# Kernel tuning notes

Hardware: AMD Instinct MI355X
Metric: run time of the kernel (lower is better)

The kernel has to match this reference:

```python
import jax, jax.numpy as jnp
import numpy as np

B, D, T, K = 16, 512, 4096, 1024

def setup_inputs() -> dict:
    key = jax.random.key(0)
    kx, kc = jax.random.split(key)
    x = jax.random.normal(kx, (B, D, T), dtype=jnp.float32)
    codebook = jax.random.normal(kc, (K, D), dtype=jnp.float32)
    return {"x": x, "codebook": codebook}

def reference(x, codebook):
    # x: [B, D, T] -> xt: [B, T, D]
    xt = jnp.transpose(x, (0, 2, 1))
    x_sq = jnp.sum(xt * xt, axis=-1, keepdims=True)          # [B, T, 1]
    c_sq = jnp.sum(codebook * codebook, axis=-1)             # [K]
    cross = jnp.einsum('btd,kd->btk', xt, codebook)          # [B, T, K]
    dist = x_sq - 2.0 * cross + c_sq                         # [B, T, K]
    indexes = jnp.argmin(dist, axis=2)                       # [B, T] int
    quantized = codebook[indexes]                            # [B, T, D]
    quantized = jnp.transpose(quantized, (0, 2, 1))          # [B, D, T]
    return quantized, indexes
```

## Files before the change

kernel.cpp:

```cpp
#include <hip/hip_runtime.h>

#define BB 16
#define DD 512
#define TT 4096
#define KK 1024

typedef _Float16 h16;
typedef __attribute__((ext_vector_type(8))) _Float16 half8;
typedef __attribute__((ext_vector_type(4))) float float4v;

#define XTH_OFF 0ull
#define XTL_OFF 67108864ull
#define CBH_OFF 134217728ull
#define CBL_OFF 135266304ull
#define CSQ_OFF 136314880ull
#define WS_NEED (136314880ull + 4096ull)

#define GLOAD_LDS16(g, l) __builtin_amdgcn_global_load_lds( \
    (const __attribute__((address_space(1))) void*)(g),      \
    (__attribute__((address_space(3))) void*)(l), 16, 0, 0)

__global__ void csq_kernel(const float* __restrict__ cb, float* __restrict__ csq) {
    int wave = threadIdx.x >> 6;
    int lane = threadIdx.x & 63;
    int row  = blockIdx.x * 4 + wave;
    const float* r = cb + (size_t)row * DD;
    float s = 0.f;
    #pragma unroll
    for (int i = 0; i < DD / 64; ++i) { float v = r[lane + i * 64]; s += v * v; }
    #pragma unroll
    for (int off = 32; off; off >>= 1) s += __shfl_down(s, off, 64);
    if (lane == 0) csq[row] = s;
}

__global__ __launch_bounds__(256) void split_x_kernel(const float* __restrict__ x,
                                                      h16* __restrict__ xth,
                                                      h16* __restrict__ xtl) {
    __shared__ float xs[32][132];
    const int tb = blockIdx.x, dcb = blockIdx.y, b = blockIdx.z;
    const int tid = threadIdx.x;
    const int t0 = tb * 128, d0 = dcb * 32;
    const float* xp = x + ((size_t)b * DD + d0) * TT + t0;
    #pragma unroll
    for (int j = 0; j < 4; ++j) {
        int i4 = tid + 256 * j;
        int dd = i4 >> 5, c4 = (i4 & 31) << 2;
        *(float4*)&xs[dd][c4] = *(const float4*)(xp + (size_t)dd * TT + c4);
    }
    __syncthreads();
    const int r = tid >> 1;
    const int ch = (tid & 1) * 16;
    h16 hv[16], lv[16];
    #pragma unroll
    for (int i = 0; i < 16; ++i) {
        float v = xs[ch + i][r];
        h16 h = (h16)v;
        hv[i] = h;
        lv[i] = (h16)(v - (float)h);
    }
    size_t o = (((size_t)(b * 32 + tb) * 16) + dcb) * 4096 + (size_t)tid * 16;
    *(half8*)(xth + o)     = *(half8*)&hv[0];
    *(half8*)(xth + o + 8) = *(half8*)&hv[8];
    *(half8*)(xtl + o)     = *(half8*)&lv[0];
    *(half8*)(xtl + o + 8) = *(half8*)&lv[8];
}

__global__ __launch_bounds__(256) void split_cb_kernel(const float* __restrict__ cb,
                                                       h16* __restrict__ cbh,
                                                       h16* __restrict__ cbl) {
    const int kb = blockIdx.x >> 4, dcb = blockIdx.x & 15;
    const int tid = threadIdx.x;
    const float* cp = cb + ((size_t)kb * 128) * DD + dcb * 32;
    h16* oh = cbh + ((size_t)(kb * 16 + dcb)) * 4096;
    h16* ol = cbl + ((size_t)(kb * 16 + dcb)) * 4096;
    #pragma unroll
    for (int j = 0; j < 4; ++j) {
        int i4 = tid + 256 * j;
        int rr = i4 >> 3, c4 = (i4 & 7) << 2;
        float4 v = *(const float4*)(cp + (size_t)rr * DD + c4);
        float vv[4] = {v.x, v.y, v.z, v.w};
        h16 h[4], l[4];
        #pragma unroll
        for (int i = 0; i < 4; ++i) {
            h[i] = (h16)vv[i];
            l[i] = (h16)(vv[i] - (float)h[i]);
        }
        *(ushort4*)(oh + rr * 32 + c4) = *(ushort4*)h;
        *(ushort4*)(ol + rr * 32 + c4) = *(ushort4*)l;
    }
}

__global__ __launch_bounds__(256, 2) void mfma_argmin_kernel(
    const h16* __restrict__ xth, const h16* __restrict__ xtl,
    const h16* __restrict__ cbh, const h16* __restrict__ cbl,
    const float* __restrict__ csq, const float* __restrict__ cb,
    float* __restrict__ idx_f_out, float* __restrict__ out) {

    __shared__ h16 ash[2][4096];
    __shared__ h16 asl[2][4096];
    __shared__ h16 bsh[2][4096];
    __shared__ h16 bsl[2][4096];
    __shared__ float redv[2][128];
    __shared__ int   redi[2][128];

    const int tid = threadIdx.x;
    const int wid = tid >> 6, lane = tid & 63;
    const int wm = wid & 1, wn = wid >> 1;
    const int tb = blockIdx.x, b = blockIdx.y;
    const int t0 = tb * 128;
    const int c  = lane & 15;
    const int q  = lane >> 4;

    const h16* aH = xth + ((size_t)(b * 32 + tb) * 16) * 4096;
    const h16* aL = xtl + ((size_t)(b * 32 + tb) * 16) * 4096;

    const int soff0 = tid * 8;
    const int soff1 = soff0 + 2048;

    GLOAD_LDS16(aH + soff0,  &ash[0][soff0]);
    GLOAD_LDS16(aH + soff1,  &ash[0][soff1]);
    GLOAD_LDS16(aL + soff0,  &asl[0][soff0]);
    GLOAD_LDS16(aL + soff1,  &asl[0][soff1]);
    GLOAD_LDS16(cbh + soff0, &bsh[0][soff0]);
    GLOAD_LDS16(cbh + soff1, &bsh[0][soff1]);
    GLOAD_LDS16(cbl + soff0, &bsl[0][soff0]);
    GLOAD_LDS16(cbl + soff1, &bsl[0][soff1]);

    float best[16];
    int   bidx[16];
    #pragma unroll
    for (int i = 0; i < 16; ++i) { best[i] = 3.4e38f; bidx[i] = 0; }

    asm volatile("s_waitcnt vmcnt(0)\n\ts_barrier" ::: "memory");

    for (int kci = 0; kci < 8; ++kci) {
        float4v acc[4][4];
        #pragma unroll
        for (int m = 0; m < 4; ++m)
            #pragma unroll
            for (int n = 0; n < 4; ++n)
                acc[m][n] = (float4v){0.f, 0.f, 0.f, 0.f};

        for (int dcb = 0; dcb < 16; ++dcb) {
            const int g  = kci * 16 + dcb;
            const int bf = g & 1;

            if (g + 1 < 128) {
                const int gn = g + 1;
                const int kn = gn >> 4, dn = gn & 15;
                const int nb = bf ^ 1;
                const h16* aHs = aH + (size_t)dn * 4096;
                const h16* aLs = aL + (size_t)dn * 4096;
                const h16* bHs = cbh + ((size_t)(kn * 16 + dn)) * 4096;
                const h16* bLs = cbl + ((size_t)(kn * 16 + dn)) * 4096;
                GLOAD_LDS16(aHs + soff0, &ash[nb][soff0]);
                GLOAD_LDS16(aHs + soff1, &ash[nb][soff1]);
                GLOAD_LDS16(aLs + soff0, &asl[nb][soff0]);
                GLOAD_LDS16(aLs + soff1, &asl[nb][soff1]);
                GLOAD_LDS16(bHs + soff0, &bsh[nb][soff0]);
                GLOAD_LDS16(bHs + soff1, &bsh[nb][soff1]);
                GLOAD_LDS16(bLs + soff0, &bsl[nb][soff0]);
                GLOAD_LDS16(bLs + soff1, &bsl[nb][soff1]);
            }

            const int doff = q * 8;
            half8 Ah[4], Al[4], Bh[4], Bl[4];
            #pragma unroll
            for (int m = 0; m < 4; ++m) {
                int row = wm * 64 + m * 16 + c;
                Ah[m] = *(const half8*)(&ash[bf][row * 32 + doff]);
                Al[m] = *(const half8*)(&asl[bf][row * 32 + doff]);
            }
            #pragma unroll
            for (int n = 0; n < 4; ++n) {
                int row = wn * 64 + n * 16 + c;
                Bh[n] = *(const half8*)(&bsh[bf][row * 32 + doff]);
                Bl[n] = *(const half8*)(&bsl[bf][row * 32 + doff]);
            }

            __builtin_amdgcn_s_setprio(1);
            #pragma unroll
            for (int n = 0; n < 4; ++n)
                #pragma unroll
                for (int m = 0; m < 4; ++m)
                    acc[m][n] = __builtin_amdgcn_mfma_f32_16x16x32_f16(Ah[m], Bh[n], acc[m][n], 0, 0, 0);
            #pragma unroll
            for (int n = 0; n < 4; ++n)
                #pragma unroll
                for (int m = 0; m < 4; ++m)
                    acc[m][n] = __builtin_amdgcn_mfma_f32_16x16x32_f16(Ah[m], Bl[n], acc[m][n], 0, 0, 0);
            #pragma unroll
            for (int n = 0; n < 4; ++n)
                #pragma unroll
                for (int m = 0; m < 4; ++m)
                    acc[m][n] = __builtin_amdgcn_mfma_f32_16x16x32_f16(Al[m], Bh[n], acc[m][n], 0, 0, 0);
            __builtin_amdgcn_s_setprio(0);

            asm volatile("s_waitcnt vmcnt(0)\n\ts_barrier" ::: "memory");
        }

        #pragma unroll
        for (int n = 0; n < 4; ++n) {
            int kg = kci * 128 + wn * 64 + n * 16 + c;
            float cq = csq[kg];
            #pragma unroll
            for (int m = 0; m < 4; ++m)
                #pragma unroll
                for (int r = 0; r < 4; ++r) {
                    float s = fmaf(-2.0f, acc[m][n][r], cq);
                    int slot = m * 4 + r;
                    if (s < best[slot]) { best[slot] = s; bidx[slot] = kg; }
                }
        }
    }

    #pragma unroll
    for (int slot = 0; slot < 16; ++slot) {
        float v = best[slot]; int i = bidx[slot];
        #pragma unroll
        for (int d = 1; d < 16; d <<= 1) {
            float pv = __shfl_xor(v, d);
            int   pi = __shfl_xor(i, d);
            if (pv < v || (pv == v && pi < i)) { v = pv; i = pi; }
        }
        if (c == 0) {
            int m = slot >> 2, r = slot & 3;
            int tl = wm * 64 + m * 16 + q * 4 + r;
            redv[wn][tl] = v; redi[wn][tl] = i;
        }
    }
    __syncthreads();
    if (tid < 128) {
        float v0 = redv[0][tid]; int i0 = redi[0][tid];
        float v1 = redv[1][tid]; int i1 = redi[1][tid];
        if (v1 < v0 || (v1 == v0 && i1 < i0)) { v0 = v1; i0 = i1; }
        idx_f_out[(size_t)b * TT + t0 + tid] = (float)i0;
        redi[0][tid] = i0;
    }
    __syncthreads();

    const int tl = tid & 127, dg = tid >> 7;
    const int k = redi[0][tl];
    const float* row = cb + (size_t)k * DD + dg * 256;
    float* ob = out + ((size_t)b * DD + dg * 256) * TT + t0 + tl;
    #pragma unroll 4
    for (int i = 0; i < 64; ++i) {
        float4 v = *(const float4*)(row + i * 4);
        ob[(size_t)(i * 4 + 0) * TT] = v.x;
        ob[(size_t)(i * 4 + 1) * TT] = v.y;
        ob[(size_t)(i * 4 + 2) * TT] = v.z;
        ob[(size_t)(i * 4 + 3) * TT] = v.w;
    }
}

__global__ void gather_kernel(const float* __restrict__ cb,
                              const float* __restrict__ idx_f,
                              float* __restrict__ out) {
    int b  = blockIdx.y;
    int t  = blockIdx.x * 256 + threadIdx.x;
    int d0 = blockIdx.z * (DD / 4);
    int k  = (int)idx_f[(size_t)b * TT + t];
    const float* row = cb + (size_t)k * DD;
    float* ob = out + (size_t)b * DD * TT + t;
    #pragma unroll 8
    for (int d = d0; d < d0 + DD / 4; ++d)
        ob[(size_t)d * TT] = row[d];
}

__global__ __launch_bounds__(256) void argmin_fp32_kernel(
    const float* __restrict__ x, const float* __restrict__ cb,
    const float* __restrict__ csq, float* __restrict__ idx_f_out) {

    __shared__ float xs[32][128];
    __shared__ float cs[32][132];

    const int tid = threadIdx.x;
    const int b = blockIdx.y;
    const int t_blk = blockIdx.x * 128;
    const int tq = tid & 15, kq = tid >> 4;
    const int t0 = tq * 8, k0 = kq * 8;
    const float* xb = x + (size_t)b * DD * TT;

    float best[8]; int bidx[8];
    #pragma unroll
    for (int i = 0; i < 8; ++i) { best[i] = 3.4e38f; bidx[i] = 0; }

    for (int kc = 0; kc < KK; kc += 128) {
        float acc[8][8];
        #pragma unroll
        for (int i = 0; i < 8; ++i)
            #pragma unroll
            for (int j = 0; j < 8; ++j) acc[i][j] = 0.f;
        for (int dc = 0; dc < DD; dc += 32) {
            __syncthreads();
            #pragma unroll
            for (int j = 0; j < 4; ++j) {
                int i4 = tid + 256 * j;
                int dd = i4 >> 5, tp = (i4 & 31) << 2;
                *(float4*)&xs[dd][tp] =
                    *(const float4*)(xb + (size_t)(dc + dd) * TT + t_blk + tp);
            }
            #pragma unroll
            for (int j = 0; j < 4; ++j) {
                int i4 = tid + 256 * j;
                int kk = i4 >> 3, dq = (i4 & 7) << 2;
                float4 v = *(const float4*)(cb + (size_t)(kc + kk) * DD + dc + dq);
                cs[dq + 0][kk] = v.x; cs[dq + 1][kk] = v.y;
                cs[dq + 2][kk] = v.z; cs[dq + 3][kk] = v.w;
            }
            __syncthreads();
            #pragma unroll 8
            for (int dd = 0; dd < 32; ++dd) {
                float a[8], bv[8];
                *(float4*)&a[0]  = *(const float4*)&xs[dd][t0];
                *(float4*)&a[4]  = *(const float4*)&xs[dd][t0 + 4];
                *(float4*)&bv[0] = *(const float4*)&cs[dd][k0];
                *(float4*)&bv[4] = *(const float4*)&cs[dd][k0 + 4];
                #pragma unroll
                for (int i = 0; i < 8; ++i)
                    #pragma unroll
                    for (int j = 0; j < 8; ++j)
                        acc[i][j] = fmaf(a[i], bv[j], acc[i][j]);
            }
        }
        #pragma unroll
        for (int j = 0; j < 8; ++j) {
            int kg = kc + k0 + j;
            float cq = csq[kg];
            #pragma unroll
            for (int i = 0; i < 8; ++i) {
                float s = cq - 2.0f * acc[i][j];
                if (s < best[i]) { best[i] = s; bidx[i] = kg; }
            }
        }
    }
    __syncthreads();
    float* rbest = &xs[0][0];
    int*   ridx  = (int*)&cs[0][0];
    #pragma unroll
    for (int i = 0; i < 8; ++i) {
        rbest[kq * 128 + t0 + i] = best[i];
        ridx [kq * 128 + t0 + i] = bidx[i];
    }
    __syncthreads();
    if (tid < 128) {
        float bv = rbest[tid]; int bi = ridx[tid];
        #pragma unroll
        for (int g = 1; g < 16; ++g) {
            float v = rbest[g * 128 + tid]; int ii = ridx[g * 128 + tid];
            if (v < bv || (v == bv && ii < bi)) { bv = v; bi = ii; }
        }
        idx_f_out[(size_t)b * TT + t_blk + tid] = (float)bi;
    }
}

extern "C" void kernel_launch(void* const* d_in, const int* in_sizes, int n_in,
                              void* d_out, int out_size, void* d_ws, size_t ws_size,
                              hipStream_t stream) {
    const float* x  = (const float*)d_in[0];
    const float* cb = (const float*)d_in[1];
    float* out   = (float*)d_out;
    float* idx_f = out + (size_t)BB * DD * TT;

    if (ws_size >= WS_NEED) {
        h16* xth = (h16*)((char*)d_ws + XTH_OFF);
        h16* xtl = (h16*)((char*)d_ws + XTL_OFF);
        h16* cbh = (h16*)((char*)d_ws + CBH_OFF);
        h16* cbl = (h16*)((char*)d_ws + CBL_OFF);
        float* csq = (float*)((char*)d_ws + CSQ_OFF);

        csq_kernel<<<KK / 4, 256, 0, stream>>>(cb, csq);
        split_cb_kernel<<<128, 256, 0, stream>>>(cb, cbh, cbl);
        split_x_kernel<<<dim3(TT / 128, DD / 32, BB), 256, 0, stream>>>(x, xth, xtl);
        mfma_argmin_kernel<<<dim3(TT / 128, BB), 256, 0, stream>>>(
            xth, xtl, cbh, cbl, csq, cb, idx_f, out);
    } else {
        float* csq = (float*)d_ws;
        csq_kernel<<<KK / 4, 256, 0, stream>>>(cb, csq);
        argmin_fp32_kernel<<<dim3(TT / 128, BB), 256, 0, stream>>>(x, cb, csq, idx_f);
        gather_kernel<<<dim3(TT / 256, BB, 4), 256, 0, stream>>>(cb, idx_f, out);
    }
}
```

Baseline: 501.4 us.

## Use 8 waves per block with halved per-wave N tile and deeper prefetch

The argmin GEMM kernel now launches 512 threads (8 waves) per block, with each wave covering 32 codebook columns instead of 64. This halves accumulator registers and lets more waves hide latency. The LDS pipeline is reworked to prefetch two stages ahead, with partial vmcnt waits and barriers placed before the MFMA block. The final cross-wave argmin reduction grows to four groups, and the gather/transposed write is split across four d-groups. The risks are the extra barriers per stage, the lower MFMA work per LDS read, and the removal of setprio.

Result: faster. 488.8 us (-2.5%).

```diff
diff --git a/kernel.cpp b/kernel.cpp
--- a/kernel.cpp
+++ b/kernel.cpp
@@ -90,7 +90,7 @@
     }
 }
 
-__global__ __launch_bounds__(256, 2) void mfma_argmin_kernel(
+__global__ __launch_bounds__(512, 4) void mfma_argmin_kernel(
     const h16* __restrict__ xth, const h16* __restrict__ xtl,
     const h16* __restrict__ cbh, const h16* __restrict__ cbl,
     const float* __restrict__ csq, const float* __restrict__ cb,
@@ -100,12 +100,13 @@
     __shared__ h16 asl[2][4096];
     __shared__ h16 bsh[2][4096];
     __shared__ h16 bsl[2][4096];
-    __shared__ float redv[2][128];
-    __shared__ int   redi[2][128];
+    __shared__ float redv[4][128];
+    __shared__ int   redi[4][128];
 
     const int tid = threadIdx.x;
     const int wid = tid >> 6, lane = tid & 63;
-    const int wm = wid & 1, wn = wid >> 1;
+    const int wm = wid & 1;
+    const int wn = wid >> 1;
     const int tb = blockIdx.x, b = blockIdx.y;
     const int t0 = tb * 128;
     const int c  = lane & 15;
@@ -114,57 +115,40 @@
     const h16* aH = xth + ((size_t)(b * 32 + tb) * 16) * 4096;
     const h16* aL = xtl + ((size_t)(b * 32 + tb) * 16) * 4096;
 
-    const int soff0 = tid * 8;
-    const int soff1 = soff0 + 2048;
-
-    GLOAD_LDS16(aH + soff0,  &ash[0][soff0]);
-    GLOAD_LDS16(aH + soff1,  &ash[0][soff1]);
-    GLOAD_LDS16(aL + soff0,  &asl[0][soff0]);
-    GLOAD_LDS16(aL + soff1,  &asl[0][soff1]);
-    GLOAD_LDS16(cbh + soff0, &bsh[0][soff0]);
-    GLOAD_LDS16(cbh + soff1, &bsh[0][soff1]);
-    GLOAD_LDS16(cbl + soff0, &bsl[0][soff0]);
-    GLOAD_LDS16(cbl + soff1, &bsl[0][soff1]);
+    const int soff = tid * 8;
+
+    GLOAD_LDS16(aH  + soff,        &ash[0][soff]);
+    GLOAD_LDS16(aL  + soff,        &asl[0][soff]);
+    GLOAD_LDS16(cbh + soff,        &bsh[0][soff]);
+    GLOAD_LDS16(cbl + soff,        &bsl[0][soff]);
+    GLOAD_LDS16(aH  + 4096 + soff, &ash[1][soff]);
+    GLOAD_LDS16(aL  + 4096 + soff, &asl[1][soff]);
+    GLOAD_LDS16(cbh + 4096 + soff, &bsh[1][soff]);
+    GLOAD_LDS16(cbl + 4096 + soff, &bsl[1][soff]);
 
     float best[16];
     int   bidx[16];
     #pragma unroll
     for (int i = 0; i < 16; ++i) { best[i] = 3.4e38f; bidx[i] = 0; }
 
-    asm volatile("s_waitcnt vmcnt(0)\n\ts_barrier" ::: "memory");
-
     for (int kci = 0; kci < 8; ++kci) {
-        float4v acc[4][4];
+        float4v acc[4][2];
         #pragma unroll
         for (int m = 0; m < 4; ++m)
             #pragma unroll
-            for (int n = 0; n < 4; ++n)
+            for (int n = 0; n < 2; ++n)
                 acc[m][n] = (float4v){0.f, 0.f, 0.f, 0.f};
 
         for (int dcb = 0; dcb < 16; ++dcb) {
             const int g  = kci * 16 + dcb;
             const int bf = g & 1;
 
-            if (g + 1 < 128) {
-                const int gn = g + 1;
-                const int kn = gn >> 4, dn = gn & 15;
-                const int nb = bf ^ 1;
-                const h16* aHs = aH + (size_t)dn * 4096;
-                const h16* aLs = aL + (size_t)dn * 4096;
-                const h16* bHs = cbh + ((size_t)(kn * 16 + dn)) * 4096;
-                const h16* bLs = cbl + ((size_t)(kn * 16 + dn)) * 4096;
-                GLOAD_LDS16(aHs + soff0, &ash[nb][soff0]);
-                GLOAD_LDS16(aHs + soff1, &ash[nb][soff1]);
-                GLOAD_LDS16(aLs + soff0, &asl[nb][soff0]);
-                GLOAD_LDS16(aLs + soff1, &asl[nb][soff1]);
-                GLOAD_LDS16(bHs + soff0, &bsh[nb][soff0]);
-                GLOAD_LDS16(bHs + soff1, &bsh[nb][soff1]);
-                GLOAD_LDS16(bLs + soff0, &bsl[nb][soff0]);
-                GLOAD_LDS16(bLs + soff1, &bsl[nb][soff1]);
-            }
+            if (g < 127) asm volatile("s_waitcnt vmcnt(4)" ::: "memory");
+            else         asm volatile("s_waitcnt vmcnt(0)" ::: "memory");
+            __builtin_amdgcn_s_barrier();
 
             const int doff = q * 8;
-            half8 Ah[4], Al[4], Bh[4], Bl[4];
+            half8 Ah[4], Al[4], Bh[2], Bl[2];
             #pragma unroll
             for (int m = 0; m < 4; ++m) {
                 int row = wm * 64 + m * 16 + c;
@@ -172,36 +156,44 @@
                 Al[m] = *(const half8*)(&asl[bf][row * 32 + doff]);
             }
             #pragma unroll
-            for (int n = 0; n < 4; ++n) {
-                int row = wn * 64 + n * 16 + c;
+            for (int n = 0; n < 2; ++n) {
+                int row = wn * 32 + n * 16 + c;
                 Bh[n] = *(const half8*)(&bsh[bf][row * 32 + doff]);
                 Bl[n] = *(const half8*)(&bsl[bf][row * 32 + doff]);
             }
 
-            __builtin_amdgcn_s_setprio(1);
-            #pragma unroll
-            for (int n = 0; n < 4; ++n)
+            asm volatile("s_waitcnt lgkmcnt(0)" ::: "memory");
+            __builtin_amdgcn_s_barrier();
+
+            if (g + 2 < 128) {
+                const int gn = g + 2;
+                const int kn = gn >> 4, dn = gn & 15;
+                GLOAD_LDS16(aH + (size_t)dn * 4096 + soff,                    &ash[bf][soff]);
+                GLOAD_LDS16(aL + (size_t)dn * 4096 + soff,                    &asl[bf][soff]);
+                GLOAD_LDS16(cbh + ((size_t)(kn * 16 + dn)) * 4096 + soff,     &bsh[bf][soff]);
+                GLOAD_LDS16(cbl + ((size_t)(kn * 16 + dn)) * 4096 + soff,     &bsl[bf][soff]);
+            }
+
+            #pragma unroll
+            for (int n = 0; n < 2; ++n)
                 #pragma unroll
                 for (int m = 0; m < 4; ++m)
                     acc[m][n] = __builtin_amdgcn_mfma_f32_16x16x32_f16(Ah[m], Bh[n], acc[m][n], 0, 0, 0);
             #pragma unroll
-            for (int n = 0; n < 4; ++n)
+            for (int n = 0; n < 2; ++n)
                 #pragma unroll
                 for (int m = 0; m < 4; ++m)
                     acc[m][n] = __builtin_amdgcn_mfma_f32_16x16x32_f16(Ah[m], Bl[n], acc[m][n], 0, 0, 0);
             #pragma unroll
-            for (int n = 0; n < 4; ++n)
+            for (int n = 0; n < 2; ++n)
                 #pragma unroll
                 for (int m = 0; m < 4; ++m)
                     acc[m][n] = __builtin_amdgcn_mfma_f32_16x16x32_f16(Al[m], Bh[n], acc[m][n], 0, 0, 0);
-            __builtin_amdgcn_s_setprio(0);
-
-            asm volatile("s_waitcnt vmcnt(0)\n\ts_barrier" ::: "memory");
-        }
-
-        #pragma unroll
-        for (int n = 0; n < 4; ++n) {
-            int kg = kci * 128 + wn * 64 + n * 16 + c;
+        }
+
+        #pragma unroll
+        for (int n = 0; n < 2; ++n) {
+            int kg = kci * 128 + wn * 32 + n * 16 + c;
             float cq = csq[kg];
             #pragma unroll
             for (int m = 0; m < 4; ++m)
@@ -232,8 +224,11 @@
     __syncthreads();
     if (tid < 128) {
         float v0 = redv[0][tid]; int i0 = redi[0][tid];
-        float v1 = redv[1][tid]; int i1 = redi[1][tid];
-        if (v1 < v0 || (v1 == v0 && i1 < i0)) { v0 = v1; i0 = i1; }
+        #pragma unroll
+        for (int gi = 1; gi < 4; ++gi) {
+            float v1 = redv[gi][tid]; int i1 = redi[gi][tid];
+            if (v1 < v0 || (v1 == v0 && i1 < i0)) { v0 = v1; i0 = i1; }
+        }
         idx_f_out[(size_t)b * TT + t0 + tid] = (float)i0;
         redi[0][tid] = i0;
     }
@@ -241,10 +236,10 @@
 
     const int tl = tid & 127, dg = tid >> 7;
     const int k = redi[0][tl];
-    const float* row = cb + (size_t)k * DD + dg * 256;
-    float* ob = out + ((size_t)b * DD + dg * 256) * TT + t0 + tl;
+    const float* row = cb + (size_t)k * DD + dg * 128;
+    float* ob = out + ((size_t)b * DD + dg * 128) * TT + t0 + tl;
     #pragma unroll 4
-    for (int i = 0; i < 64; ++i) {
+    for (int i = 0; i < 32; ++i) {
         float4 v = *(const float4*)(row + i * 4);
         ob[(size_t)(i * 4 + 0) * TT] = v.x;
         ob[(size_t)(i * 4 + 1) * TT] = v.y;
@@ -372,7 +367,7 @@
         csq_kernel<<<KK / 4, 256, 0, stream>>>(cb, csq);
         split_cb_kernel<<<128, 256, 0, stream>>>(cb, cbh, cbl);
         split_x_kernel<<<dim3(TT / 128, DD / 32, BB), 256, 0, stream>>>(x, xth, xtl);
-        mfma_argmin_kernel<<<dim3(TT / 128, BB), 256, 0, stream>>>(
+        mfma_argmin_kernel<<<dim3(TT / 128, BB), 512, 0, stream>>>(
             xth, xtl, cbh, cbl, csq, cb, idx_f, out);
     } else {
         float* csq = (float*)d_ws;
```
